# Kernel tuning notes

Measured on AMD Instinct MI355X. Metric: run time of the kernel, lower is better.

## Reference

```python
import jax, jax.numpy as jnp
import numpy as np

N, MA, F, NF = 512, 64, 128, 16
UPDATE_RATIO = 0.1
DECAY = 1.0
EPS = 1e-12  # avoids NaN grad of sqrt at self-distance 0 (torch diagonal is masked out by exp anyway)


def setup_inputs() -> dict:
    key = jax.random.key(0)
    ks = jax.random.split(key, 8)
    z = jax.random.randint(ks[0], (N, MA), 0, 10, dtype=jnp.int64) if jax.config.jax_enable_x64 else jax.random.randint(ks[0], (N, MA), 0, 10, dtype=jnp.int32)
    # pad last few atoms of each molecule with -1 to exercise the mask
    z = z.at[:, MA - 8:].set(-1)
    r = jax.random.normal(ks[1], (N, MA, 3), dtype=jnp.float32) * 3.0
    h = jax.random.normal(ks[2], (N, MA, F), dtype=jnp.float32)
    distances = jnp.linspace(0.5, 6.0, NF, dtype=jnp.float32)
    widths = jax.random.uniform(ks[3], (NF,), dtype=jnp.float32) * 0.5 + 0.5  # keep sigma > 0
    din = F * (1 + NF)  # 2176
    W1 = jax.random.normal(ks[4], (din, 512), dtype=jnp.float32) * (1.0 / np.sqrt(din))
    b1 = jnp.zeros((512,), dtype=jnp.float32)
    W2 = jax.random.normal(ks[5], (512, F), dtype=jnp.float32) * (1.0 / np.sqrt(512.0))
    b2 = jnp.zeros((F,), dtype=jnp.float32)
    return {"z": z, "r": r, "h": h, "distances": distances, "widths": widths,
            "W1": W1, "b1": b1, "W2": W2, "b2": b2}


def reference(z, r, h, distances, widths, W1, b1, W2, b2):
    n, ma = z.shape
    nf = distances.shape[0]
    # pairwise distance: (n, ma, ma)
    dv = r[:, :, None, :] - r[:, None, :, :]
    d = jnp.sqrt(jnp.sum(dv * dv, axis=-1) + EPS)
    mu = distances.reshape(1, nf, 1, 1)
    sigma = widths.reshape(1, nf, 1, 1)
    mask1 = (z > -1).astype(h.dtype)                      # (n, ma)
    pair_mask = mask1[:, :, None] * mask1[:, None, :]     # (n, ma, ma)
    # Gaussian RBF scores, masked: (n, nf, ma, ma)
    w = pair_mask[:, None] * jnp.exp(-((d[:, None] - mu) ** 2) / sigma) * 5.0
    # aggregate neighbor features: (n, ma, nf, F) -> (n, ma, nf*F)
    u = jnp.einsum('nfab,nbc->nafc', w, h).reshape(n, ma, nf * h.shape[-1])
    v = jnp.concatenate([h, u], axis=2)                   # (n, ma, F*(1+nf))
    v = jax.nn.silu(v @ W1 + b1) @ W2 + b2                # MLP 'net'
    h_new = h + v * UPDATE_RATIO * DECAY * mask1[:, :, None]
    return (z, r, h_new)
```

## Files before the change

kernel.cpp:

```cpp
#include <hip/hip_runtime.h>

#define MA 64
#define F 128
#define NF 16
#define HID 512
#define LDUB 136
#define UBSZ 8704
#define WLB  17408
#define WLSZ 9216
#define LDWB 144
#define LDT1B 528

typedef float  float4v __attribute__((ext_vector_type(4)));
typedef short  short8  __attribute__((ext_vector_type(8)));

static __device__ __forceinline__ unsigned int pack2bf(float x, float y) {
    unsigned int a = __float_as_uint(x) + 0x8000u;
    unsigned int b = __float_as_uint(y) + 0x8000u;
    return __builtin_amdgcn_perm(b, a, 0x07060302u);
}
static __device__ __forceinline__ unsigned short f2bf1(float x) {
    return (unsigned short)((__float_as_uint(x) + 0x8000u) >> 16);
}
static __device__ __forceinline__ unsigned int pk4fp8(float a, float b, float c, float d) {
    int p = __builtin_amdgcn_cvt_pk_fp8_f32(a, b, 0, false);
    p = __builtin_amdgcn_cvt_pk_fp8_f32(c, d, p, true);
    return (unsigned int)p;
}

__global__ void pack_frags(const float* __restrict__ W1, const float* __restrict__ W2,
                           unsigned char* __restrict__ w1p, unsigned char* __restrict__ w2p) {
    int gid  = blockIdx.x * 4 + (threadIdx.x >> 6);
    int lane = threadIdx.x & 63;
    int kq   = (lane >> 4) * 8;
    int arow = lane & 15;
    float v[8];
    if (gid < 68 * 32) {
        int kt = gid >> 5, jt = gid & 31;
        const float* base = W1 + (size_t)(kt * 32 + kq) * HID + jt * 16 + arow;
        #pragma unroll
        for (int j = 0; j < 8; j++) v[j] = base[j * HID];
        uint2 o = { pk4fp8(v[0], v[1], v[2], v[3]), pk4fp8(v[4], v[5], v[6], v[7]) };
        *(uint2*)(w1p + ((size_t)gid * 64 + lane) * 8) = o;
    } else {
        int g2 = gid - 68 * 32;
        int kt = g2 >> 3, mt = g2 & 7;
        const float* base = W2 + (size_t)(kt * 32 + kq) * F + mt * 16 + arow;
        #pragma unroll
        for (int j = 0; j < 8; j++) v[j] = base[j * F];
        uint2 o = { pk4fp8(v[0], v[1], v[2], v[3]), pk4fp8(v[4], v[5], v[6], v[7]) };
        *(uint2*)(w2p + ((size_t)g2 * 64 + lane) * 8) = o;
    }
}

__launch_bounds__(512, 2)
__global__ void node_conv_mfma(const int* __restrict__ z, const float* __restrict__ rr,
        const float* __restrict__ h, const float* __restrict__ dist,
        const float* __restrict__ wid, const float* __restrict__ b1,
        const float* __restrict__ b2,
        const unsigned char* __restrict__ w1p, const unsigned char* __restrict__ w2p,
        float* __restrict__ out) {
    const int nb = blockIdx.x;
    const int tid = threadIdx.x;
    const int lane = tid & 63;
    const int wave = tid >> 6;
    const int arow = lane & 15;
    const int quad = lane >> 4;
    const int kgrp = quad * 8;

    __shared__ __attribute__((aligned(16))) unsigned char lds[35840];
    __shared__ float r_lds[2][MA][4];

    const int N = gridDim.x * 2;
    const int n0 = nb * 2;
    const float* hg0 = h + (size_t)n0 * MA * F;

    if (tid < 2 * MA) {
        int zi = z[n0 * MA + tid];
        out[(size_t)n0 * MA + tid] = (float)zi;
        int mol = tid >> 6, a = tid & 63;
        r_lds[mol][a][0] = rr[(n0 * MA + tid) * 3 + 0];
        r_lds[mol][a][1] = rr[(n0 * MA + tid) * 3 + 1];
        r_lds[mol][a][2] = rr[(n0 * MA + tid) * 3 + 2];
        r_lds[mol][a][3] = (zi > -1) ? 1.0f : 0.0f;
    }
    if (tid < 2 * MA * 3)
        out[(size_t)N * MA + (size_t)n0 * MA * 3 + tid] = rr[(size_t)n0 * MA * 3 + tid];

    for (int i = tid; i < 2 * MA * F / 4; i += 512) {
        float4 v = ((const float4*)hg0)[i];
        int mol = i >> 11;
        int j = i & 2047;
        int a = j >> 5, c4 = (j & 31) * 4;
        *(unsigned int*)&lds[mol * UBSZ + a * LDUB + c4] = pk4fp8(v.x, v.y, v.z, v.w);
    }
    short8 ah[2][2];
    {
        int c = wave * 16 + arow;
        #pragma unroll
        for (int mol = 0; mol < 2; mol++) {
            const float* hm = hg0 + mol * MA * F;
            #pragma unroll
            for (int ks2 = 0; ks2 < 2; ks2++)
                #pragma unroll
                for (int j = 0; j < 8; j++)
                    ah[mol][ks2][j] = (short)f2bf1(hm[(size_t)(ks2 * 32 + kgrp + j) * F + c]);
        }
    }
    __syncthreads();

    const int wa = tid >> 3;
    const int wb0 = (tid & 7) * 8;
    float dpre[2][8];
    #pragma unroll
    for (int mol = 0; mol < 2; mol++) {
        float ax = r_lds[mol][wa][0], ay = r_lds[mol][wa][1], az = r_lds[mol][wa][2];
        float am = r_lds[mol][wa][3];
        #pragma unroll
        for (int j = 0; j < 8; j++) {
            float dx = ax - r_lds[mol][wb0 + j][0];
            float dy = ay - r_lds[mol][wb0 + j][1];
            float dz = az - r_lds[mol][wb0 + j][2];
            float d = sqrtf(dx * dx + dy * dy + dz * dz + 1e-12f);
            float mm = am * r_lds[mol][wb0 + j][3];
            dpre[mol][j] = d + (1.0f - mm) * 1e4f;
        }
    }

    {
        float mu = dist[0];
        float isg = 1.0f / wid[0];
        #pragma unroll
        for (int mol = 0; mol < 2; mol++) {
            float e[8];
            #pragma unroll
            for (int j = 0; j < 8; j++) {
                float t = dpre[mol][j] - mu;
                e[j] = 5.0f * __expf(-t * t * isg);
            }
            uint4 wp = { pack2bf(e[0], e[1]), pack2bf(e[2], e[3]),
                         pack2bf(e[4], e[5]), pack2bf(e[6], e[7]) };
            *(uint4*)&lds[WLB + mol * WLSZ + wa * LDWB + wb0 * 2] = wp;
        }
    }
    long afr[2][4];
    {
        const unsigned char* p = w1p + ((size_t)(wave * 4) * 64 + lane) * 8;
        #pragma unroll
        for (int mt = 0; mt < 4; mt++) afr[0][mt] = *(const long*)(p + mt * 512);
    }
    __syncthreads();

    const float4v zf = {0.f, 0.f, 0.f, 0.f};
    float4v acc[2][4][4];
    #pragma unroll
    for (int m = 0; m < 2; m++)
        #pragma unroll
        for (int i = 0; i < 4; i++)
            #pragma unroll
            for (int jv = 0; jv < 4; jv++) acc[m][i][jv] = zf;

    for (int f = 0; f <= NF; f++) {
        const unsigned char* pA = w1p + (((size_t)(f * 128) + wave * 4) * 64 + lane) * 8;

        long bfr[2][2][4];
        #pragma unroll
        for (int mol = 0; mol < 2; mol++)
            #pragma unroll
            for (int at = 0; at < 4; at++)
                bfr[0][mol][at] = *(const long*)&lds[mol * UBSZ + (at * 16 + arow) * LDUB + kgrp];
        #pragma unroll
        for (int ks = 0; ks < 4; ks++) {
            long* acur = afr[ks & 1];
            long* anxt = afr[(ks + 1) & 1];
            {
                const unsigned char* pN = (ks < 3) ? (pA + (ks + 1) * 16384)
                                                   : (pA + ((f < NF) ? 65536 : 0));
                #pragma unroll
                for (int mt = 0; mt < 4; mt++) anxt[mt] = *(const long*)(pN + mt * 512);
            }
            long (*bcur)[4] = bfr[ks & 1];
            long (*bnxt)[4] = bfr[(ks + 1) & 1];
            if (ks < 3) {
                #pragma unroll
                for (int mol = 0; mol < 2; mol++)
                    #pragma unroll
                    for (int at = 0; at < 4; at++)
                        bnxt[mol][at] = *(const long*)&lds[mol * UBSZ + (at * 16 + arow) * LDUB + (ks + 1) * 32 + kgrp];
            }
            #pragma unroll
            for (int mt = 0; mt < 4; mt++)
                #pragma unroll
                for (int mol = 0; mol < 2; mol++)
                    #pragma unroll
                    for (int at = 0; at < 4; at++)
                        acc[mol][mt][at] = __builtin_amdgcn_mfma_f32_16x16x32_fp8_fp8(
                            acur[mt], bcur[mol][at], acc[mol][mt][at], 0, 0, 0);
        }

        unsigned int udp[2][4];
        if (f < NF) {
            #pragma unroll
            for (int mol = 0; mol < 2; mol++) {
                float4v ud[4];
                #pragma unroll
                for (int at = 0; at < 4; at++) ud[at] = zf;
                #pragma unroll
                for (int ks2 = 0; ks2 < 2; ks2++)
                    #pragma unroll
                    for (int at = 0; at < 4; at++) {
                        short8 bw = *(const short8*)&lds[WLB + mol * WLSZ + (at * 16 + arow) * LDWB + (ks2 * 32 + kgrp) * 2];
                        ud[at] = __builtin_amdgcn_mfma_f32_16x16x32_bf16(ah[mol][ks2], bw, ud[at], 0, 0, 0);
                    }
                #pragma unroll
                for (int at = 0; at < 4; at++)
                    udp[mol][at] = pk4fp8(ud[at][0], ud[at][1], ud[at][2], ud[at][3]);
            }
        }
        __syncthreads();

        if (f < NF) {
            #pragma unroll
            for (int mol = 0; mol < 2; mol++)
                #pragma unroll
                for (int at = 0; at < 4; at++)
                    *(unsigned int*)&lds[mol * UBSZ + (at * 16 + arow) * LDUB + wave * 16 + quad * 4] = udp[mol][at];

            if (f <= NF - 2) {
                float mu = dist[f + 1];
                float isg = 1.0f / wid[f + 1];
                #pragma unroll
                for (int mol = 0; mol < 2; mol++) {
                    float e[8];
                    #pragma unroll
                    for (int j = 0; j < 8; j++) {
                        float t = dpre[mol][j] - mu;
                        e[j] = 5.0f * __expf(-t * t * isg);
                    }
                    uint4 wp = { pack2bf(e[0], e[1]), pack2bf(e[2], e[3]),
                                 pack2bf(e[4], e[5]), pack2bf(e[6], e[7]) };
                    *(uint4*)&lds[WLB + mol * WLSZ + wa * LDWB + wb0 * 2] = wp;
                }
            }
            __syncthreads();
        }
    }

    float4 b1v[4];
    #pragma unroll
    for (int mt = 0; mt < 4; mt++)
        b1v[mt] = *(const float4*)&b1[wave * 64 + mt * 16 + quad * 4];
    float* outh0 = out + (size_t)N * MA * 4 + (size_t)n0 * MA * F;

    #pragma unroll
    for (int half = 0; half < 4; half++) {
        const int mol = half >> 1, hh = half & 1;
        if (half) __syncthreads();
        #pragma unroll
        for (int mt = 0; mt < 4; mt++) {
            #pragma unroll
            for (int ai = 0; ai < 2; ai++) {
                const int at = hh * 2 + ai;
                float xs[4];
                #pragma unroll
                for (int r = 0; r < 4; r++) {
                    float x = acc[mol][mt][at][r] + ((const float*)&b1v[mt])[r];
                    xs[r] = x / (1.0f + __expf(-x));
                }
                *(unsigned int*)&lds[(ai * 16 + arow) * LDT1B + wave * 64 + mt * 16 + quad * 4] =
                    pk4fp8(xs[0], xs[1], xs[2], xs[3]);
            }
        }
        __syncthreads();

        float4v g2[2] = {zf, zf};
        for (int ks = 0; ks < 16; ks++) {
            long aw2 = *(const long*)(w2p + ((size_t)(ks * 8 + wave) * 64 + lane) * 8);
            #pragma unroll
            for (int n2 = 0; n2 < 2; n2++) {
                long bt = *(const long*)&lds[(n2 * 16 + arow) * LDT1B + ks * 32 + kgrp];
                g2[n2] = __builtin_amdgcn_mfma_f32_16x16x32_fp8_fp8(aw2, bt, g2[n2], 0, 0, 0);
            }
        }
        const float* hgm = hg0 + mol * MA * F;
        float* outh = outh0 + mol * MA * F;
        #pragma unroll
        for (int n2 = 0; n2 < 2; n2++) {
            int a = hh * 32 + n2 * 16 + arow;
            int c0 = wave * 16 + quad * 4;
            float m = r_lds[mol][a][3] * 0.1f;
            float4 hv = *(const float4*)&hgm[a * F + c0];
            float4 b2v = *(const float4*)&b2[c0];
            float4 res;
            res.x = hv.x + (g2[n2][0] + b2v.x) * m;
            res.y = hv.y + (g2[n2][1] + b2v.y) * m;
            res.z = hv.z + (g2[n2][2] + b2v.z) * m;
            res.w = hv.w + (g2[n2][3] + b2v.w) * m;
            *(float4*)&outh[(size_t)a * F + c0] = res;
        }
    }
}

extern "C" void kernel_launch(void* const* d_in, const int* in_sizes, int n_in,
                              void* d_out, int out_size, void* d_ws, size_t ws_size,
                              hipStream_t stream) {
    const int*   z    = (const int*)d_in[0];
    const float* rr   = (const float*)d_in[1];
    const float* h    = (const float*)d_in[2];
    const float* dist = (const float*)d_in[3];
    const float* wid  = (const float*)d_in[4];
    const float* W1   = (const float*)d_in[5];
    const float* b1   = (const float*)d_in[6];
    const float* W2   = (const float*)d_in[7];
    const float* b2   = (const float*)d_in[8];
    float* out = (float*)d_out;

    int Nmol = in_sizes[0] / MA;

    unsigned char* w1p = (unsigned char*)d_ws;
    unsigned char* w2p = w1p + (size_t)68 * 32 * 64 * 8;

    pack_frags<<<576, 256, 0, stream>>>(W1, W2, w1p, w2p);
    node_conv_mfma<<<Nmol / 2, 512, 0, stream>>>(z, rr, h, dist, wid, b1, b2, w1p, w2p, out);
}
```

Measured before the change: 159.5 us.

## Switch first GEMM to 16x16x128 scaled FP8 MFMA and second GEMM to bf16

The W1 GEMM now uses the gfx950 scaled MFMA with K=128 per instruction, so it needs wider 32-byte A/B fragments. The weight packing and the LDS U-buffer stride are relaid out to match, and the software-pipelined per-k-step prefetch is replaced by one weight fetch per feature block. The goal is to issue fewer, larger matrix instructions and fewer loads. The second GEMM moves from fp8 to bf16 for W2 and the hidden activations, which raises accuracy but doubles LDS and weight bytes there. Dropping the fine-grained prefetch may expose load latency.

```diff
diff --git a/kernel.cpp b/kernel.cpp
--- a/kernel.cpp
+++ b/kernel.cpp
@@ -4,15 +4,16 @@
 #define F 128
 #define NF 16
 #define HID 512
-#define LDUB 136
-#define UBSZ 8704
-#define WLB  17408
+#define LDUB 144
+#define UBSZ 9216
+#define WLB  18432
 #define WLSZ 9216
 #define LDWB 144
-#define LDT1B 528
+#define LDT1B 1040
 
 typedef float  float4v __attribute__((ext_vector_type(4)));
 typedef short  short8  __attribute__((ext_vector_type(8)));
+typedef int    int8v   __attribute__((ext_vector_type(8)));
 
 static __device__ __forceinline__ unsigned int pack2bf(float x, float y) {
     unsigned int a = __float_as_uint(x) + 0x8000u;
@@ -29,27 +30,30 @@
 }
 
 __global__ void pack_frags(const float* __restrict__ W1, const float* __restrict__ W2,
-                           unsigned char* __restrict__ w1p, unsigned char* __restrict__ w2p) {
+                           unsigned char* __restrict__ w1p, unsigned short* __restrict__ w2p) {
     int gid  = blockIdx.x * 4 + (threadIdx.x >> 6);
     int lane = threadIdx.x & 63;
-    int kq   = (lane >> 4) * 8;
     int arow = lane & 15;
-    float v[8];
-    if (gid < 68 * 32) {
+    int kq   = lane >> 4;
+    if (gid < 544) {
         int kt = gid >> 5, jt = gid & 31;
-        const float* base = W1 + (size_t)(kt * 32 + kq) * HID + jt * 16 + arow;
-        #pragma unroll
-        for (int j = 0; j < 8; j++) v[j] = base[j * HID];
-        uint2 o = { pk4fp8(v[0], v[1], v[2], v[3]), pk4fp8(v[4], v[5], v[6], v[7]) };
-        *(uint2*)(w1p + ((size_t)gid * 64 + lane) * 8) = o;
-    } else {
-        int g2 = gid - 68 * 32;
+        const float* base = W1 + (size_t)(kt * 128 + kq * 32) * HID + jt * 16 + arow;
+        unsigned int o[8];
+        #pragma unroll
+        for (int p = 0; p < 8; p++)
+            o[p] = pk4fp8(base[(p * 4 + 0) * HID], base[(p * 4 + 1) * HID],
+                          base[(p * 4 + 2) * HID], base[(p * 4 + 3) * HID]);
+        unsigned char* dst = w1p + ((size_t)gid * 64 + lane) * 32;
+        *(uint4*)dst        = (uint4){o[0], o[1], o[2], o[3]};
+        *(uint4*)(dst + 16) = (uint4){o[4], o[5], o[6], o[7]};
+    } else if (gid < 544 + 128) {
+        int g2 = gid - 544;
         int kt = g2 >> 3, mt = g2 & 7;
-        const float* base = W2 + (size_t)(kt * 32 + kq) * F + mt * 16 + arow;
-        #pragma unroll
-        for (int j = 0; j < 8; j++) v[j] = base[j * F];
-        uint2 o = { pk4fp8(v[0], v[1], v[2], v[3]), pk4fp8(v[4], v[5], v[6], v[7]) };
-        *(uint2*)(w2p + ((size_t)g2 * 64 + lane) * 8) = o;
+        const float* base = W2 + (size_t)(kt * 32 + kq * 8) * F + mt * 16 + arow;
+        short8 o;
+        #pragma unroll
+        for (int j = 0; j < 8; j++) o[j] = (short)f2bf1(base[j * F]);
+        *(short8*)(w2p + ((size_t)g2 * 64 + lane) * 8) = o;
     }
 }
 
@@ -58,7 +62,7 @@
         const float* __restrict__ h, const float* __restrict__ dist,
         const float* __restrict__ wid, const float* __restrict__ b1,
         const float* __restrict__ b2,
-        const unsigned char* __restrict__ w1p, const unsigned char* __restrict__ w2p,
+        const unsigned char* __restrict__ w1p, const unsigned short* __restrict__ w2p,
         float* __restrict__ out) {
     const int nb = blockIdx.x;
     const int tid = threadIdx.x;
@@ -68,7 +72,7 @@
     const int quad = lane >> 4;
     const int kgrp = quad * 8;
 
-    __shared__ __attribute__((aligned(16))) unsigned char lds[35840];
+    __shared__ __attribute__((aligned(16))) unsigned char lds[36864];
     __shared__ float r_lds[2][MA][4];
 
     const int N = gridDim.x * 2;
@@ -143,12 +147,10 @@
             *(uint4*)&lds[WLB + mol * WLSZ + wa * LDWB + wb0 * 2] = wp;
         }
     }
-    long afr[2][4];
-    {
-        const unsigned char* p = w1p + ((size_t)(wave * 4) * 64 + lane) * 8;
-        #pragma unroll
-        for (int mt = 0; mt < 4; mt++) afr[0][mt] = *(const long*)(p + mt * 512);
-    }
+    int8v afr[4];
+    #pragma unroll
+    for (int mt = 0; mt < 4; mt++)
+        afr[mt] = *(const int8v*)(w1p + ((size_t)((wave * 4 + mt) * 64 + lane)) * 32);
     __syncthreads();
 
     const float4v zf = {0.f, 0.f, 0.f, 0.f};
@@ -161,42 +163,16 @@
             for (int jv = 0; jv < 4; jv++) acc[m][i][jv] = zf;
 
     for (int f = 0; f <= NF; f++) {
-        const unsigned char* pA = w1p + (((size_t)(f * 128) + wave * 4) * 64 + lane) * 8;
-
-        long bfr[2][2][4];
         #pragma unroll
         for (int mol = 0; mol < 2; mol++)
             #pragma unroll
-            for (int at = 0; at < 4; at++)
-                bfr[0][mol][at] = *(const long*)&lds[mol * UBSZ + (at * 16 + arow) * LDUB + kgrp];
-        #pragma unroll
-        for (int ks = 0; ks < 4; ks++) {
-            long* acur = afr[ks & 1];
-            long* anxt = afr[(ks + 1) & 1];
-            {
-                const unsigned char* pN = (ks < 3) ? (pA + (ks + 1) * 16384)
-                                                   : (pA + ((f < NF) ? 65536 : 0));
-                #pragma unroll
-                for (int mt = 0; mt < 4; mt++) anxt[mt] = *(const long*)(pN + mt * 512);
-            }
-            long (*bcur)[4] = bfr[ks & 1];
-            long (*bnxt)[4] = bfr[(ks + 1) & 1];
-            if (ks < 3) {
-                #pragma unroll
-                for (int mol = 0; mol < 2; mol++)
-                    #pragma unroll
-                    for (int at = 0; at < 4; at++)
-                        bnxt[mol][at] = *(const long*)&lds[mol * UBSZ + (at * 16 + arow) * LDUB + (ks + 1) * 32 + kgrp];
-            }
-            #pragma unroll
-            for (int mt = 0; mt < 4; mt++)
-                #pragma unroll
-                for (int mol = 0; mol < 2; mol++)
-                    #pragma unroll
-                    for (int at = 0; at < 4; at++)
-                        acc[mol][mt][at] = __builtin_amdgcn_mfma_f32_16x16x32_fp8_fp8(
-                            acur[mt], bcur[mol][at], acc[mol][mt][at], 0, 0, 0);
-        }
+            for (int at = 0; at < 4; at++) {
+                int8v bfr = *(const int8v*)&lds[mol * UBSZ + (at * 16 + arow) * LDUB + quad * 32];
+                #pragma unroll
+                for (int mt = 0; mt < 4; mt++)
+                    acc[mol][mt][at] = __builtin_amdgcn_mfma_scale_f32_16x16x128_f8f6f4(
+                        afr[mt], bfr, acc[mol][mt][at], 0, 0, 0, 127, 0, 127);
+            }
 
         unsigned int udp[2][4];
         if (f < NF) {
@@ -220,6 +196,10 @@
         __syncthreads();
 
         if (f < NF) {
+            const unsigned char* pN = w1p + ((size_t)(((f + 1) * 32 + wave * 4) * 64 + lane)) * 32;
+            #pragma unroll
+            for (int mt = 0; mt < 4; mt++) afr[mt] = *(const int8v*)(pN + mt * 2048);
+
             #pragma unroll
             for (int mol = 0; mol < 2; mol++)
                 #pragma unroll
@@ -267,19 +247,19 @@
                     float x = acc[mol][mt][at][r] + ((const float*)&b1v[mt])[r];
                     xs[r] = x / (1.0f + __expf(-x));
                 }
-                *(unsigned int*)&lds[(ai * 16 + arow) * LDT1B + wave * 64 + mt * 16 + quad * 4] =
-                    pk4fp8(xs[0], xs[1], xs[2], xs[3]);
+                uint2 pv = { pack2bf(xs[0], xs[1]), pack2bf(xs[2], xs[3]) };
+                *(uint2*)&lds[(ai * 16 + arow) * LDT1B + (wave * 64 + mt * 16 + quad * 4) * 2] = pv;
             }
         }
         __syncthreads();
 
         float4v g2[2] = {zf, zf};
         for (int ks = 0; ks < 16; ks++) {
-            long aw2 = *(const long*)(w2p + ((size_t)(ks * 8 + wave) * 64 + lane) * 8);
+            short8 aw2 = *(const short8*)(w2p + ((size_t)(ks * 8 + wave) * 64 + lane) * 8);
             #pragma unroll
             for (int n2 = 0; n2 < 2; n2++) {
-                long bt = *(const long*)&lds[(n2 * 16 + arow) * LDT1B + ks * 32 + kgrp];
-                g2[n2] = __builtin_amdgcn_mfma_f32_16x16x32_fp8_fp8(aw2, bt, g2[n2], 0, 0, 0);
+                short8 bt = *(const short8*)&lds[(n2 * 16 + arow) * LDT1B + (ks * 32 + kgrp) * 2];
+                g2[n2] = __builtin_amdgcn_mfma_f32_16x16x32_bf16(aw2, bt, g2[n2], 0, 0, 0);
             }
         }
         const float* hgm = hg0 + mol * MA * F;
@@ -317,9 +297,9 @@
 
     int Nmol = in_sizes[0] / MA;
 
-    unsigned char* w1p = (unsigned char*)d_ws;
-    unsigned char* w2p = w1p + (size_t)68 * 32 * 64 * 8;
-
-    pack_frags<<<576, 256, 0, stream>>>(W1, W2, w1p, w2p);
+    unsigned char*  w1p = (unsigned char*)d_ws;
+    unsigned short* w2p = (unsigned short*)(w1p + (size_t)544 * 64 * 32);
+
+    pack_frags<<<168, 256, 0, stream>>>(W1, W2, w1p, w2p);
     node_conv_mfma<<<Nmol / 2, 512, 0, stream>>>(z, rr, h, dist, wid, b1, b2, w1p, w2p, out);
 }
```

Measured after the change: 201.7 us. 1.26x slower.
